# Performance work log

Measured on AMD Instinct MI355X. Metric: run time of the kernel, lower is better.

## Reference

```python
import jax, jax.numpy as jnp
import numpy as np

B, N, D, P, H, DH = 1, 1536, 512, 64, 16, 64
INNER = H * DH  # 1024

def _ln(x, g, b, eps=1e-5):
    m = jnp.mean(x, axis=-1, keepdims=True)
    v = jnp.var(x, axis=-1, keepdims=True)
    return (x - m) / jnp.sqrt(v + eps) * g + b

def setup_inputs() -> dict:
    key = jax.random.key(0)
    ks = jax.random.split(key, 10)
    s = 0.02
    return {
        "node_feats": jax.random.normal(ks[0], (B, N, D), jnp.float32),
        "pair_feats": jax.random.normal(ks[1], (B, N, N, P), jnp.float32),
        "mask": jnp.ones((B, N, N), dtype=bool),
        "ln_node_g": jnp.ones((D,), jnp.float32), "ln_node_b": jnp.zeros((D,), jnp.float32),
        "ln_pair_g": jnp.ones((P,), jnp.float32), "ln_pair_b": jnp.zeros((P,), jnp.float32),
        "Wq": s * jax.random.normal(ks[2], (D, INNER), jnp.float32),
        "bq": jnp.zeros((INNER,), jnp.float32),
        "Wkv": s * jax.random.normal(ks[3], (D, 2 * INNER), jnp.float32),
        "bkv": jnp.zeros((2 * INNER,), jnp.float32),
        "qln_g": jnp.ones((INNER,), jnp.float32), "qln_b": jnp.zeros((INNER,), jnp.float32),
        "kln_g": jnp.ones((INNER,), jnp.float32), "kln_b": jnp.zeros((INNER,), jnp.float32),
        "Wg": s * jax.random.normal(ks[4], (D, INNER), jnp.float32),
        "bg": jnp.zeros((INNER,), jnp.float32),
        "Wbias": s * jax.random.normal(ks[5], (P, H), jnp.float32),
        "Wout": s * jax.random.normal(ks[6], (INNER, D), jnp.float32),
        "bout": jnp.zeros((D,), jnp.float32),
        "n_queries": 0,
        "n_keys": 0,
    }

def reference(node_feats, pair_feats, mask, ln_node_g, ln_node_b, ln_pair_g, ln_pair_b,
              Wq, bq, Wkv, bkv, qln_g, qln_b, kln_g, kln_b, Wg, bg, Wbias, Wout, bout,
              n_queries, n_keys):
    b, n, _ = node_feats.shape
    x = _ln(node_feats, ln_node_g, ln_node_b)          # [b,n,D]
    p = _ln(pair_feats, ln_pair_g, ln_pair_b)          # [b,n,n,P]
    q = _ln(x @ Wq + bq, qln_g, qln_b)                 # [b,n,I]
    kv = x @ Wkv + bkv
    k, v = jnp.split(kv, 2, axis=-1)
    k = _ln(k, kln_g, kln_b)
    g = x @ Wg + bg                                    # gating, [b,n,I]
    bias = jnp.einsum('bijp,ph->bhij', p, Wbias)       # pair bias, [b,h,n,n]
    # split heads -> [b,h,n,dh]
    split = lambda t: t.reshape(b, n, H, DH).transpose(0, 2, 1, 3)
    qh, kh, vh, gh = split(q), split(k), split(v), split(g)
    scale = DH ** -0.5
    sim = jnp.einsum('bhid,bhjd->bhij', qh, kh) * scale
    sim = jnp.where(mask[:, None, :, :], sim, jnp.finfo(sim.dtype).min)
    attn = jax.nn.softmax(sim + bias, axis=-1)
    o = jnp.einsum('bhij,bhjd->bhid', attn, vh)        # [b,h,n,dh]
    o = jax.nn.sigmoid(gh) * o
    o = o.transpose(0, 2, 1, 3).reshape(b, n, INNER)
    return o @ Wout + bout
```

## Files before the change

kernel.cpp:

```cpp
#include <hip/hip_runtime.h>

#define NN 1536
#define DD 512
#define PP 64
#define HH 16
#define DHD 64
#define INNER 1024
#define NCHUNK 4
#define JT_PER 6

typedef __attribute__((ext_vector_type(4))) float f32x4;
typedef __attribute__((ext_vector_type(8))) _Float16 f16x8;
typedef __attribute__((ext_vector_type(4))) _Float16 f16x4;

__device__ inline float wave_sum(float v) {
#pragma unroll
  for (int m = 1; m <= 32; m <<= 1) v += __shfl_xor(v, m);
  return v;
}

__global__ __launch_bounds__(256) void prep_kernel(const float* __restrict__ Wq,
    const float* __restrict__ Wkv, const float* __restrict__ Wg,
    const float* __restrict__ Wout, const float* __restrict__ nf,
    const float* __restrict__ lng, const float* __restrict__ lnb,
    _Float16* __restrict__ BTall, _Float16* __restrict__ WoutT,
    _Float16* __restrict__ x16) {
  int bid = blockIdx.x;
  int tid = threadIdx.x;
  if (bid >= 640) {
    int i = bid - 640;
    int c = tid * 2;
    float2 v = *(const float2*)&nf[(size_t)i * DD + c];
    float s = v.x + v.y, ss = v.x * v.x + v.y * v.y;
    s = wave_sum(s); ss = wave_sum(ss);
    __shared__ float red[2][4];
    int w = tid >> 6;
    if ((tid & 63) == 0) { red[0][w] = s; red[1][w] = ss; }
    __syncthreads();
    s = red[0][0] + red[0][1] + red[0][2] + red[0][3];
    ss = red[1][0] + red[1][1] + red[1][2] + red[1][3];
    float mean = s * (1.f / DD);
    float var = ss * (1.f / DD) - mean * mean;
    float rstd = rsqrtf(var + 1e-5f);
    x16[(size_t)i * DD + c + 0] = (_Float16)((v.x - mean) * rstd * lng[c + 0] + lnb[c + 0]);
    x16[(size_t)i * DD + c + 1] = (_Float16)((v.y - mean) * rstd * lng[c + 1] + lnb[c + 1]);
    return;
  }
  const float* src; int Cs, c0, r0, outStride, outCol; _Float16* dst;
  if (bid < 512) {
    int x = bid & 63, y = bid >> 6;
    int cg0 = x * 64; r0 = y * 64;
    if (cg0 < 1024)      { src = Wq;  Cs = 1024; c0 = cg0; }
    else if (cg0 < 3072) { src = Wkv; Cs = 2048; c0 = cg0 - 1024; }
    else                 { src = Wg;  Cs = 1024; c0 = cg0 - 3072; }
    dst = BTall; outStride = DD; outCol = cg0;
  } else {
    int b = bid - 512;
    int x = b & 7, y = b >> 3;
    c0 = x * 64; r0 = y * 64;
    src = Wout; Cs = DD; dst = WoutT; outStride = INNER; outCol = c0;
  }
  __shared__ float tile[64][65];
  int ri = tid >> 4, ci = (tid & 15) * 4;
#pragma unroll
  for (int p = 0; p < 4; ++p) {
    float4 v = *(const float4*)&src[(size_t)(r0 + ri + p * 16) * Cs + c0 + ci];
    tile[ri + p * 16][ci + 0] = v.x;
    tile[ri + p * 16][ci + 1] = v.y;
    tile[ri + p * 16][ci + 2] = v.z;
    tile[ri + p * 16][ci + 3] = v.w;
  }
  __syncthreads();
  int wr = tid >> 3, wc = (tid & 7) * 8;
#pragma unroll
  for (int p = 0; p < 2; ++p) {
    f16x8 o;
#pragma unroll
    for (int jj = 0; jj < 8; ++jj) o[jj] = (_Float16)tile[wc + jj][wr + p * 32];
    *(f16x8*)&dst[(size_t)(outCol + wr + p * 32) * outStride + r0 + wc] = o;
  }
}

__device__ __forceinline__ void pb_body(int i, int q, int tid,
    const float* __restrict__ pair, const float* __restrict__ pg,
    const float* __restrict__ pb, const float* __restrict__ Wbias,
    _Float16* __restrict__ bias16) {
  int lane = tid & 63, w = tid >> 6;
  int lj = lane & 15, pbase = (lane >> 4) * 8;
  const int off0 = 0, off1 = 4, off2 = 32, off3 = 36;
  f16x8 wb0, wb1;
#pragma unroll
  for (int jj = 0; jj < 8; ++jj) {
    wb0[jj] = (_Float16)Wbias[(pbase + jj) * HH + lj];
    wb1[jj] = (_Float16)Wbias[(pbase + 32 + jj) * HH + lj];
  }
  f32x4 gv0 = *(const f32x4*)&pg[pbase + off0], gv1 = *(const f32x4*)&pg[pbase + off1];
  f32x4 gv2 = *(const f32x4*)&pg[pbase + off2], gv3 = *(const f32x4*)&pg[pbase + off3];
  f32x4 bb0 = *(const f32x4*)&pb[pbase + off0], bb1 = *(const f32x4*)&pb[pbase + off1];
  f32x4 bb2 = *(const f32x4*)&pb[pbase + off2], bb3 = *(const f32x4*)&pb[pbase + off3];
  __shared__ _Float16 trans[2][16][72];
  int jbase = q * 384 + w * 16 + lj;
  const float* srcp = &pair[((size_t)i * NN + jbase) * PP];
  f32x4 v0 = *(const f32x4*)&srcp[pbase + off0];
  f32x4 v1 = *(const f32x4*)&srcp[pbase + off1];
  f32x4 v2 = *(const f32x4*)&srcp[pbase + off2];
  f32x4 v3 = *(const f32x4*)&srcp[pbase + off3];
  for (int t = 0; t < 6; ++t) {
    int jt0 = q * 384 + t * 64;
    f32x4 n0, n1, n2, n3;
    if (t < 5) {
      const float* ns = &pair[((size_t)i * NN + jbase + (t + 1) * 64) * PP];
      n0 = *(const f32x4*)&ns[pbase + off0];
      n1 = *(const f32x4*)&ns[pbase + off1];
      n2 = *(const f32x4*)&ns[pbase + off2];
      n3 = *(const f32x4*)&ns[pbase + off3];
    }
    float s = 0.f, ss = 0.f;
#pragma unroll
    for (int e = 0; e < 4; ++e) {
      s += v0[e] + v1[e] + v2[e] + v3[e];
      ss += v0[e] * v0[e] + v1[e] * v1[e] + v2[e] * v2[e] + v3[e] * v3[e];
    }
    s += __shfl_xor(s, 16); s += __shfl_xor(s, 32);
    ss += __shfl_xor(ss, 16); ss += __shfl_xor(ss, 32);
    float mean = s * (1.f / PP);
    float var = ss * (1.f / PP) - mean * mean;
    float rstd = rsqrtf(var + 1e-5f);
    f16x8 a0, a1;
#pragma unroll
    for (int e = 0; e < 4; ++e) {
      a0[e]     = (_Float16)((v0[e] - mean) * rstd * gv0[e] + bb0[e]);
      a0[4 + e] = (_Float16)((v1[e] - mean) * rstd * gv1[e] + bb1[e]);
      a1[e]     = (_Float16)((v2[e] - mean) * rstd * gv2[e] + bb2[e]);
      a1[4 + e] = (_Float16)((v3[e] - mean) * rstd * gv3[e] + bb3[e]);
    }
    f32x4 cacc = {};
    cacc = __builtin_amdgcn_mfma_f32_16x16x32_f16(a0, wb0, cacc, 0, 0, 0);
    cacc = __builtin_amdgcn_mfma_f32_16x16x32_f16(a1, wb1, cacc, 0, 0, 0);
#pragma unroll
    for (int rg = 0; rg < 4; ++rg)
      trans[t & 1][lj][w * 16 + (lane >> 4) * 4 + rg] = (_Float16)cacc[rg];
    __syncthreads();
    int hh = tid >> 4, jc = (tid & 15) * 4;
    f16x4 ov = *(const f16x4*)&trans[t & 1][hh][jc];
    *(f16x4*)&bias16[((size_t)hh * NN + i) * NN + jt0 + jc] = ov;
    v0 = n0; v1 = n1; v2 = n2; v3 = n3;
  }
}

__device__ __forceinline__ void gemm_proj_body(int m0, int n0, int tid,
    const _Float16* __restrict__ A, const _Float16* __restrict__ BT,
    const float* __restrict__ bq, const float* __restrict__ bkv,
    const float* __restrict__ bg, _Float16* __restrict__ C) {
  __shared__ _Float16 As[64][72];
  __shared__ _Float16 Bs[64][72];
  int lane = tid & 63, w = tid >> 6;
  int wm = (w & 1) * 32, wn = (w >> 1) * 32;
  f32x4 acc[2][2] = {};
  int r = tid >> 3, c8 = (tid & 7) * 8;
  int lr = lane & 15, lg = lane >> 4;
  for (int k0 = 0; k0 < DD; k0 += 64) {
    *(f16x8*)&As[r][c8]      = *(const f16x8*)&A[(size_t)(m0 + r) * DD + k0 + c8];
    *(f16x8*)&As[r + 32][c8] = *(const f16x8*)&A[(size_t)(m0 + r + 32) * DD + k0 + c8];
    *(f16x8*)&Bs[r][c8]      = *(const f16x8*)&BT[(size_t)(n0 + r) * DD + k0 + c8];
    *(f16x8*)&Bs[r + 32][c8] = *(const f16x8*)&BT[(size_t)(n0 + r + 32) * DD + k0 + c8];
    __syncthreads();
#pragma unroll
    for (int kf = 0; kf < 2; ++kf) {
      f16x8 a0 = *(const f16x8*)&As[wm + lr][kf * 32 + lg * 8];
      f16x8 a1 = *(const f16x8*)&As[wm + 16 + lr][kf * 32 + lg * 8];
      f16x8 b0 = *(const f16x8*)&Bs[wn + lr][kf * 32 + lg * 8];
      f16x8 b1 = *(const f16x8*)&Bs[wn + 16 + lr][kf * 32 + lg * 8];
      acc[0][0] = __builtin_amdgcn_mfma_f32_16x16x32_f16(a0, b0, acc[0][0], 0, 0, 0);
      acc[0][1] = __builtin_amdgcn_mfma_f32_16x16x32_f16(a0, b1, acc[0][1], 0, 0, 0);
      acc[1][0] = __builtin_amdgcn_mfma_f32_16x16x32_f16(a1, b0, acc[1][0], 0, 0, 0);
      acc[1][1] = __builtin_amdgcn_mfma_f32_16x16x32_f16(a1, b1, acc[1][1], 0, 0, 0);
    }
    __syncthreads();
  }
#pragma unroll
  for (int mi = 0; mi < 2; ++mi)
#pragma unroll
    for (int ni = 0; ni < 2; ++ni)
#pragma unroll
      for (int rg = 0; rg < 4; ++rg) {
        int row = m0 + wm + mi * 16 + lg * 4 + rg;
        int col = n0 + wn + ni * 16 + lr;
        float bv = (col < 1024) ? bq[col] : (col < 3072) ? bkv[col - 1024] : bg[col - 3072];
        C[(size_t)row * 4096 + col] = (_Float16)(acc[mi][ni][rg] + bv);
      }
}

__device__ __forceinline__ void qkv_body(int i, int tid,
    const _Float16* __restrict__ prebuf,
    const float* __restrict__ qg, const float* __restrict__ qb,
    const float* __restrict__ kg, const float* __restrict__ kb,
    _Float16* __restrict__ q16, _Float16* __restrict__ k16) {
  int c = tid * 4;
  const _Float16* rowp = &prebuf[(size_t)i * 4096];
  f16x4 qh = *(const f16x4*)&rowp[c];
  f16x4 kh = *(const f16x4*)&rowp[1024 + c];
  float qv[4], kv[4];
#pragma unroll
  for (int e = 0; e < 4; ++e) { qv[e] = (float)qh[e]; kv[e] = (float)kh[e]; }
  float qs = qv[0] + qv[1] + qv[2] + qv[3];
  float qss = qv[0] * qv[0] + qv[1] * qv[1] + qv[2] * qv[2] + qv[3] * qv[3];
  float ks = kv[0] + kv[1] + kv[2] + kv[3];
  float kss = kv[0] * kv[0] + kv[1] * kv[1] + kv[2] * kv[2] + kv[3] * kv[3];
  qs = wave_sum(qs); qss = wave_sum(qss); ks = wave_sum(ks); kss = wave_sum(kss);
  __shared__ float red[4][4];
  int w = tid >> 6;
  if ((tid & 63) == 0) { red[0][w] = qs; red[1][w] = qss; red[2][w] = ks; red[3][w] = kss; }
  __syncthreads();
  qs = red[0][0] + red[0][1] + red[0][2] + red[0][3];
  qss = red[1][0] + red[1][1] + red[1][2] + red[1][3];
  ks = red[2][0] + red[2][1] + red[2][2] + red[2][3];
  kss = red[3][0] + red[3][1] + red[3][2] + red[3][3];
  float qm = qs * (1.f / INNER), qvr = qss * (1.f / INNER) - qm * qm, qr = rsqrtf(qvr + 1e-5f);
  float km = ks * (1.f / INNER), kvr = kss * (1.f / INNER) - km * km, kr = rsqrtf(kvr + 1e-5f);
  int hh = c >> 6, d = c & 63;
  size_t offo = ((size_t)hh * NN + i) * DHD + d;
  f16x4 qo, ko;
#pragma unroll
  for (int e = 0; e < 4; ++e) {
    qo[e] = (_Float16)((qv[e] - qm) * qr * qg[c + e] + qb[c + e]);
    ko[e] = (_Float16)((kv[e] - km) * kr * kg[c + e] + kb[c + e]);
  }
  *(f16x4*)&q16[offo] = qo;
  *(f16x4*)&k16[offo] = ko;
}

__device__ __forceinline__ void vt_body(int t, int tid,
    const _Float16* __restrict__ prebuf, _Float16* __restrict__ vT16) {
  int z = t / 24, y = t - z * 24;
  __shared__ _Float16 tile[64][72];
  int r0 = y * 64;
  int ri = tid >> 3, ci = (tid & 7) * 8;
#pragma unroll
  for (int p = 0; p < 2; ++p)
    *(f16x8*)&tile[ri + p * 32][ci] =
        *(const f16x8*)&prebuf[(size_t)(r0 + ri + p * 32) * 4096 + 2048 + z * 64 + ci];
  __syncthreads();
#pragma unroll
  for (int p = 0; p < 2; ++p) {
    f16x8 o;
#pragma unroll
    for (int jj = 0; jj < 8; ++jj) o[jj] = tile[ci + jj][ri + p * 32];
    *(f16x8*)&vT16[((size_t)z * DHD + ri + p * 32) * NN + r0 + ci] = o;
  }
}

__device__ __forceinline__ void attn_core(int it, int h, int ck, int tid,
    const _Float16* __restrict__ q16, const _Float16* __restrict__ k16,
    const _Float16* __restrict__ vT16, const _Float16* __restrict__ bias16,
    f32x4 oacc[4], float& mOut, float& lOut) {
  int lane = tid & 63, w = tid >> 6;
  int lr = lane & 15, lg = lane >> 4;
  __shared__ _Float16 Kt[64][72];
  __shared__ _Float16 Vt[64][72];
  int ib0 = it * 64;
  int ib = ib0 + w * 16;
  f16x8 qb0 = *(const f16x8*)&q16[((size_t)h * NN + ib + lr) * DHD + lg * 8];
  f16x8 qb1 = *(const f16x8*)&q16[((size_t)h * NN + ib + lr) * DHD + 32 + lg * 8];
  float m = -INFINITY, lsum = 0.f;
  int sr = tid >> 3, sc = (tid & 7) * 8;
  int jt0g = ck * JT_PER;
  const _Float16* brow = &bias16[((size_t)h * NN + ib + lr) * NN];
  f16x8 kA, kB, vA, vB;
  {
    int j0 = jt0g * 64;
    kA = *(const f16x8*)&k16[((size_t)h * NN + j0 + sr) * DHD + sc];
    kB = *(const f16x8*)&k16[((size_t)h * NN + j0 + sr + 32) * DHD + sc];
    vA = *(const f16x8*)&vT16[((size_t)h * DHD + sr) * NN + j0 + sc];
    vB = *(const f16x8*)&vT16[((size_t)h * DHD + sr + 32) * NN + j0 + sc];
  }
  for (int jj = 0; jj < JT_PER; ++jj) {
    int j0 = (jt0g + jj) * 64;
    *(f16x8*)&Kt[sr][sc] = kA;
    *(f16x8*)&Kt[sr + 32][sc] = kB;
    *(f16x8*)&Vt[sr][sc] = vA;
    *(f16x8*)&Vt[sr + 32][sc] = vB;
    f16x4 bl[4];
#pragma unroll
    for (int jq = 0; jq < 4; ++jq)
      bl[jq] = *(const f16x4*)&brow[j0 + jq * 16 + lg * 4];
    __syncthreads();
    if (jj + 1 < JT_PER) {
      int j1 = j0 + 64;
      kA = *(const f16x8*)&k16[((size_t)h * NN + j1 + sr) * DHD + sc];
      kB = *(const f16x8*)&k16[((size_t)h * NN + j1 + sr + 32) * DHD + sc];
      vA = *(const f16x8*)&vT16[((size_t)h * DHD + sr) * NN + j1 + sc];
      vB = *(const f16x8*)&vT16[((size_t)h * DHD + sr + 32) * NN + j1 + sc];
    }
    float s[4][4];
#pragma unroll
    for (int jq = 0; jq < 4; ++jq) {
      f16x8 ka0 = *(const f16x8*)&Kt[jq * 16 + lr][lg * 8];
      f16x8 ka1 = *(const f16x8*)&Kt[jq * 16 + lr][32 + lg * 8];
      f32x4 c = {};
      c = __builtin_amdgcn_mfma_f32_16x16x32_f16(ka0, qb0, c, 0, 0, 0);
      c = __builtin_amdgcn_mfma_f32_16x16x32_f16(ka1, qb1, c, 0, 0, 0);
#pragma unroll
      for (int r = 0; r < 4; ++r)
        s[jq][r] = c[r] * 0.125f + (float)bl[jq][r];
    }
    float tmax = s[0][0];
#pragma unroll
    for (int jq = 0; jq < 4; ++jq)
#pragma unroll
      for (int r = 0; r < 4; ++r) tmax = fmaxf(tmax, s[jq][r]);
    tmax = fmaxf(tmax, __shfl_xor(tmax, 16));
    tmax = fmaxf(tmax, __shfl_xor(tmax, 32));
    float mn = fmaxf(m, tmax);
    float alpha = __expf(m - mn);
    float ps = 0.f;
    f16x4 pf[4];
#pragma unroll
    for (int jq = 0; jq < 4; ++jq)
#pragma unroll
      for (int r = 0; r < 4; ++r) {
        float p = __expf(s[jq][r] - mn);
        ps += p;
        pf[jq][r] = (_Float16)p;
      }
    ps += __shfl_xor(ps, 16);
    ps += __shfl_xor(ps, 32);
    lsum = lsum * alpha + ps;
    m = mn;
    float ar[4];
#pragma unroll
    for (int r = 0; r < 4; ++r) ar[r] = __shfl(alpha, lg * 4 + r);
#pragma unroll
    for (int dt = 0; dt < 4; ++dt)
#pragma unroll
      for (int r = 0; r < 4; ++r) oacc[dt][r] *= ar[r];
#pragma unroll
    for (int dt = 0; dt < 4; ++dt)
#pragma unroll
      for (int jq = 0; jq < 4; ++jq) {
        f16x4 vb = *(const f16x4*)&Vt[dt * 16 + lr][jq * 16 + lg * 4];
        oacc[dt] = __builtin_amdgcn_mfma_f32_16x16x16f16(pf[jq], vb, oacc[dt], 0, 0, 0);
      }
    __syncthreads();
  }
  mOut = m;
  lOut = lsum;
}

__device__ __forceinline__ void attn_body(int it, int h, int ck, int tid,
    const _Float16* __restrict__ q16, const _Float16* __restrict__ k16,
    const _Float16* __restrict__ vT16, const _Float16* __restrict__ bias16,
    _Float16* __restrict__ opart, float* __restrict__ mlbuf) {
  int lane = tid & 63, w = tid >> 6;
  int lr = lane & 15, lg = lane >> 4;
  f32x4 oacc[4] = {};
  float m, lsum;
  attn_core(it, h, ck, tid, q16, k16, vT16, bias16, oacc, m, lsum);
  size_t pbase = (((size_t)it * HH + h) * NCHUNK + ck) * 4096 + (size_t)w * 1024;
#pragma unroll
  for (int dt = 0; dt < 4; ++dt) {
    f16x4 ov;
#pragma unroll
    for (int r = 0; r < 4; ++r) ov[r] = (_Float16)oacc[dt][r];
    *(f16x4*)&opart[pbase + dt * 256 + lane * 4] = ov;
  }
  if (lg == 0) {
    size_t mb = (((size_t)it * HH + h) * NCHUNK + ck) * 128;
    mlbuf[mb + w * 16 + lr] = m;
    mlbuf[mb + 64 + w * 16 + lr] = lsum;
  }
}

__global__ __launch_bounds__(256) void fat2(const float* __restrict__ pair,
    const float* __restrict__ pg, const float* __restrict__ pb,
    const float* __restrict__ Wbias, _Float16* __restrict__ bias16,
    const _Float16* __restrict__ x16, const _Float16* __restrict__ BTall,
    const float* __restrict__ bq, const float* __restrict__ bkv,
    const float* __restrict__ bg, _Float16* __restrict__ prebuf16) {
  int bid = blockIdx.x;
  int g = bid / 3, r = bid - g * 3;
  int tid = threadIdx.x;
  if (r == 2) {
    gemm_proj_body((g >> 6) * 64, (g & 63) * 64, tid, x16, BTall, bq, bkv, bg, prebuf16);
  } else {
    int p = g * 2 + r;
    pb_body(p % NN, p / NN, tid, pair, pg, pb, Wbias, bias16);
  }
}

__global__ __launch_bounds__(256) void fat3(const float* __restrict__ pair,
    const float* __restrict__ pg, const float* __restrict__ pb,
    const float* __restrict__ Wbias, _Float16* __restrict__ bias16,
    const _Float16* __restrict__ prebuf16,
    const float* __restrict__ qg, const float* __restrict__ qb,
    const float* __restrict__ kg, const float* __restrict__ kb,
    _Float16* __restrict__ q16, _Float16* __restrict__ k16,
    _Float16* __restrict__ vT16) {
  int bid = blockIdx.x;
  int g = bid / 9, r = bid - g * 9;
  int tid = threadIdx.x;
  if (r < 4) {
    pb_body(g * 4 + r, 2, tid, pair, pg, pb, Wbias, bias16);
  } else if (r < 8) {
    qkv_body(g * 4 + (r - 4), tid, prebuf16, qg, qb, kg, kb, q16, k16);
  } else {
    vt_body(g, tid, prebuf16, vT16);
  }
}

__global__ __launch_bounds__(256) void fat4(const float* __restrict__ pair,
    const float* __restrict__ pg, const float* __restrict__ pb,
    const float* __restrict__ Wbias, _Float16* __restrict__ bias16,
    const _Float16* __restrict__ q16, const _Float16* __restrict__ k16,
    const _Float16* __restrict__ vT16, _Float16* __restrict__ opart,
    float* __restrict__ mlbuf) {
  int bid = blockIdx.x;
  int g = bid / 7, r = bid - g * 7;
  int tid = threadIdx.x;
  if (r < 4) {
    pb_body(g * 4 + r, 3, tid, pair, pg, pb, Wbias, bias16);
  } else {
    int a = g * 3 + (r - 4);
    int ck = a % 3, h = (a / 3) % 16, it = a / 48;
    attn_body(it, h, ck, tid, q16, k16, vT16, bias16, opart, mlbuf);
  }
}

__global__ __launch_bounds__(256) void attn_final(const _Float16* __restrict__ q16,
    const _Float16* __restrict__ k16, const _Float16* __restrict__ vT16,
    const _Float16* __restrict__ bias16, const _Float16* __restrict__ opart,
    const float* __restrict__ mlbuf, const _Float16* __restrict__ prebuf,
    _Float16* __restrict__ o16) {
  int it = blockIdx.x, h = blockIdx.y;
  int tid = threadIdx.x, lane = tid & 63, w = tid >> 6;
  int lr = lane & 15, lg = lane >> 4;
  f32x4 oacc[4] = {};
  float m3, l3;
  attn_core(it, h, 3, tid, q16, k16, vT16, bias16, oacc, m3, l3);
  float mc[NCHUNK], lc[NCHUNK];
#pragma unroll
  for (int c = 0; c < 3; ++c) {
    size_t mb = (((size_t)it * HH + h) * NCHUNK + c) * 128;
    mc[c] = mlbuf[mb + w * 16 + lr];
    lc[c] = mlbuf[mb + 64 + w * 16 + lr];
  }
  mc[3] = m3; lc[3] = l3;
  float mg = fmaxf(fmaxf(mc[0], mc[1]), fmaxf(mc[2], mc[3]));
  float wcc[NCHUNK], lt = 0.f;
#pragma unroll
  for (int c = 0; c < NCHUNK; ++c) {
    wcc[c] = __expf(mc[c] - mg);
    lt += wcc[c] * lc[c];
  }
  float wq[NCHUNK][4], ltq[4];
#pragma unroll
  for (int r = 0; r < 4; ++r) {
    ltq[r] = __shfl(lt, lg * 4 + r);
#pragma unroll
    for (int c = 0; c < NCHUNK; ++c) wq[c][r] = __shfl(wcc[c], lg * 4 + r);
  }
#pragma unroll
  for (int dt = 0; dt < 4; ++dt) {
    float o[4];
#pragma unroll
    for (int r = 0; r < 4; ++r) o[r] = wq[3][r] * oacc[dt][r];
#pragma unroll
    for (int c = 0; c < 3; ++c) {
      size_t base = (((size_t)it * HH + h) * NCHUNK + c) * 4096 + (size_t)w * 1024;
      f16x4 v = *(const f16x4*)&opart[base + dt * 256 + lane * 4];
#pragma unroll
      for (int r = 0; r < 4; ++r) o[r] += wq[c][r] * (float)v[r];
    }
    int d = dt * 16 + lr;
#pragma unroll
    for (int r = 0; r < 4; ++r) {
      int i = it * 64 + w * 16 + lg * 4 + r;
      float gt = (float)prebuf[(size_t)i * 4096 + 3072 + h * DHD + d];
      float val = o[r] / ltq[r] * (1.f / (1.f + __expf(-gt)));
      o16[(size_t)i * INNER + h * DHD + d] = (_Float16)val;
    }
  }
}

__global__ __launch_bounds__(256) void gemm_f16(const _Float16* __restrict__ A,
    const _Float16* __restrict__ BT, const float* __restrict__ bias,
    float* __restrict__ C, int M, int N, int K) {
  __shared__ _Float16 As[64][72];
  __shared__ _Float16 Bs[64][72];
  int tid = threadIdx.x, lane = tid & 63, w = tid >> 6;
  int m0 = blockIdx.y * 64, n0 = blockIdx.x * 64;
  int wm = (w & 1) * 32, wn = (w >> 1) * 32;
  f32x4 acc[2][2] = {};
  int r = tid >> 3, c8 = (tid & 7) * 8;
  int lr = lane & 15, lg = lane >> 4;
  for (int k0 = 0; k0 < K; k0 += 64) {
    *(f16x8*)&As[r][c8]      = *(const f16x8*)&A[(size_t)(m0 + r) * K + k0 + c8];
    *(f16x8*)&As[r + 32][c8] = *(const f16x8*)&A[(size_t)(m0 + r + 32) * K + k0 + c8];
    *(f16x8*)&Bs[r][c8]      = *(const f16x8*)&BT[(size_t)(n0 + r) * K + k0 + c8];
    *(f16x8*)&Bs[r + 32][c8] = *(const f16x8*)&BT[(size_t)(n0 + r + 32) * K + k0 + c8];
    __syncthreads();
#pragma unroll
    for (int kf = 0; kf < 2; ++kf) {
      f16x8 a0 = *(const f16x8*)&As[wm + lr][kf * 32 + lg * 8];
      f16x8 a1 = *(const f16x8*)&As[wm + 16 + lr][kf * 32 + lg * 8];
      f16x8 b0 = *(const f16x8*)&Bs[wn + lr][kf * 32 + lg * 8];
      f16x8 b1 = *(const f16x8*)&Bs[wn + 16 + lr][kf * 32 + lg * 8];
      acc[0][0] = __builtin_amdgcn_mfma_f32_16x16x32_f16(a0, b0, acc[0][0], 0, 0, 0);
      acc[0][1] = __builtin_amdgcn_mfma_f32_16x16x32_f16(a0, b1, acc[0][1], 0, 0, 0);
      acc[1][0] = __builtin_amdgcn_mfma_f32_16x16x32_f16(a1, b0, acc[1][0], 0, 0, 0);
      acc[1][1] = __builtin_amdgcn_mfma_f32_16x16x32_f16(a1, b1, acc[1][1], 0, 0, 0);
    }
    __syncthreads();
  }
#pragma unroll
  for (int mi = 0; mi < 2; ++mi)
#pragma unroll
    for (int ni = 0; ni < 2; ++ni)
#pragma unroll
      for (int rg = 0; rg < 4; ++rg) {
        int row = m0 + wm + mi * 16 + lg * 4 + rg;
        int col = n0 + wn + ni * 16 + lr;
        C[(size_t)row * N + col] = acc[mi][ni][rg] + bias[col];
      }
}

extern "C" void kernel_launch(void* const* d_in, const int* in_sizes, int n_in,
                              void* d_out, int out_size, void* d_ws, size_t ws_size,
                              hipStream_t stream) {
  const float* node  = (const float*)d_in[0];
  const float* pair  = (const float*)d_in[1];
  const float* ln_ng = (const float*)d_in[3];
  const float* ln_nb = (const float*)d_in[4];
  const float* ln_pg = (const float*)d_in[5];
  const float* ln_pb = (const float*)d_in[6];
  const float* Wq    = (const float*)d_in[7];
  const float* bq    = (const float*)d_in[8];
  const float* Wkv   = (const float*)d_in[9];
  const float* bkv   = (const float*)d_in[10];
  const float* qlg   = (const float*)d_in[11];
  const float* qlb   = (const float*)d_in[12];
  const float* klg   = (const float*)d_in[13];
  const float* klb   = (const float*)d_in[14];
  const float* Wg    = (const float*)d_in[15];
  const float* bg    = (const float*)d_in[16];
  const float* Wbias = (const float*)d_in[17];
  const float* Wout  = (const float*)d_in[18];
  const float* bout  = (const float*)d_in[19];
  float* out = (float*)d_out;

  char* ws = (char*)d_ws;
  const size_t MB = 1u << 20;
  _Float16* BTall    = (_Float16*)(ws + 0 * MB);
  _Float16* WoutT    = (_Float16*)(ws + 4 * MB);
  _Float16* x16      = (_Float16*)(ws + 5 * MB);
  _Float16* prebuf16 = (_Float16*)(ws + 8 * MB);
  _Float16* q16      = (_Float16*)(ws + 20 * MB);
  _Float16* k16      = (_Float16*)(ws + 23 * MB);
  _Float16* vT16     = (_Float16*)(ws + 29 * MB);
  _Float16* o16      = (_Float16*)(ws + 32 * MB);
  _Float16* bias16   = (_Float16*)(ws + 36 * MB);
  _Float16* opart    = (_Float16*)(ws + 112 * MB);
  float*    mlbuf    = (float*)(ws + 126 * MB);

  prep_kernel<<<640 + NN, 256, 0, stream>>>(Wq, Wkv, Wg, Wout, node, ln_ng, ln_nb,
                                            BTall, WoutT, x16);
  fat2<<<4608, 256, 0, stream>>>(pair, ln_pg, ln_pb, Wbias, bias16,
                                 x16, BTall, bq, bkv, bg, prebuf16);
  fat3<<<3456, 256, 0, stream>>>(pair, ln_pg, ln_pb, Wbias, bias16,
                                 prebuf16, qlg, qlb, klg, klb, q16, k16, vT16);
  fat4<<<2688, 256, 0, stream>>>(pair, ln_pg, ln_pb, Wbias, bias16,
                                 q16, k16, vT16, opart, mlbuf);
  attn_final<<<dim3(NN / 64, HH), 256, 0, stream>>>(q16, k16, vT16, bias16,
                                                    opart, mlbuf, prebuf16, o16);
  gemm_f16<<<dim3(DD / 64, NN / 64), 256, 0, stream>>>(o16, WoutT, bout, out, NN, DD, INNER);
}
```

Before: 242.0 us.

## Overlap pair-bias chunk with prep stage by fusing into new fat1 kernel

Turns the weight-transpose and node-layernorm prep kernel into a device function and interleaves it with pair-bias blocks in a new fat1 launch. Pair-bias chunk 0 now runs alongside prep instead of inside fat2, and fat2 shrinks to pair-bias chunk 1 plus the projection GEMM. The aim is to spread the memory-bound pair-feature streaming over more stages so it overlaps the short prep work. This rebalances the work across the pipeline. Correctness depends on the 128*29 block grid covering all 2176 prep blocks and 1536 bias rows exactly.

```diff
diff --git a/kernel.cpp b/kernel.cpp
--- a/kernel.cpp
+++ b/kernel.cpp
@@ -19,16 +19,14 @@
   return v;
 }
 
-__global__ __launch_bounds__(256) void prep_kernel(const float* __restrict__ Wq,
-    const float* __restrict__ Wkv, const float* __restrict__ Wg,
-    const float* __restrict__ Wout, const float* __restrict__ nf,
-    const float* __restrict__ lng, const float* __restrict__ lnb,
-    _Float16* __restrict__ BTall, _Float16* __restrict__ WoutT,
-    _Float16* __restrict__ x16) {
-  int bid = blockIdx.x;
-  int tid = threadIdx.x;
-  if (bid >= 640) {
-    int i = bid - 640;
+__device__ __forceinline__ void prep_body(int pid, int tid,
+    const float* __restrict__ Wq, const float* __restrict__ Wkv,
+    const float* __restrict__ Wg, const float* __restrict__ Wout,
+    const float* __restrict__ nf, const float* __restrict__ lng,
+    const float* __restrict__ lnb, _Float16* __restrict__ BTall,
+    _Float16* __restrict__ WoutT, _Float16* __restrict__ x16) {
+  if (pid >= 640) {
+    int i = pid - 640;
     int c = tid * 2;
     float2 v = *(const float2*)&nf[(size_t)i * DD + c];
     float s = v.x + v.y, ss = v.x * v.x + v.y * v.y;
@@ -47,15 +45,15 @@
     return;
   }
   const float* src; int Cs, c0, r0, outStride, outCol; _Float16* dst;
-  if (bid < 512) {
-    int x = bid & 63, y = bid >> 6;
+  if (pid < 512) {
+    int x = pid & 63, y = pid >> 6;
     int cg0 = x * 64; r0 = y * 64;
     if (cg0 < 1024)      { src = Wq;  Cs = 1024; c0 = cg0; }
     else if (cg0 < 3072) { src = Wkv; Cs = 2048; c0 = cg0 - 1024; }
     else                 { src = Wg;  Cs = 1024; c0 = cg0 - 3072; }
     dst = BTall; outStride = DD; outCol = cg0;
   } else {
-    int b = bid - 512;
+    int b = pid - 512;
     int x = b & 7, y = b >> 3;
     c0 = x * 64; r0 = y * 64;
     src = Wout; Cs = DD; dst = WoutT; outStride = INNER; outCol = c0;
@@ -371,6 +369,25 @@
   }
 }
 
+__global__ __launch_bounds__(256) void fat1(const float* __restrict__ Wq,
+    const float* __restrict__ Wkv, const float* __restrict__ Wg,
+    const float* __restrict__ Wout, const float* __restrict__ nf,
+    const float* __restrict__ lng, const float* __restrict__ lnb,
+    _Float16* __restrict__ BTall, _Float16* __restrict__ WoutT,
+    _Float16* __restrict__ x16,
+    const float* __restrict__ pair, const float* __restrict__ pg,
+    const float* __restrict__ pb, const float* __restrict__ Wbias,
+    _Float16* __restrict__ bias16) {
+  int bid = blockIdx.x;
+  int g = bid / 29, r = bid - g * 29;
+  int tid = threadIdx.x;
+  if (r < 17) {
+    prep_body(g * 17 + r, tid, Wq, Wkv, Wg, Wout, nf, lng, lnb, BTall, WoutT, x16);
+  } else {
+    pb_body(g * 12 + (r - 17), 0, tid, pair, pg, pb, Wbias, bias16);
+  }
+}
+
 __global__ __launch_bounds__(256) void fat2(const float* __restrict__ pair,
     const float* __restrict__ pg, const float* __restrict__ pb,
     const float* __restrict__ Wbias, _Float16* __restrict__ bias16,
@@ -378,13 +395,12 @@
     const float* __restrict__ bq, const float* __restrict__ bkv,
     const float* __restrict__ bg, _Float16* __restrict__ prebuf16) {
   int bid = blockIdx.x;
-  int g = bid / 3, r = bid - g * 3;
+  int g = bid >> 1, r = bid & 1;
   int tid = threadIdx.x;
-  if (r == 2) {
+  if (r == 1) {
     gemm_proj_body((g >> 6) * 64, (g & 63) * 64, tid, x16, BTall, bq, bkv, bg, prebuf16);
   } else {
-    int p = g * 2 + r;
-    pb_body(p % NN, p / NN, tid, pair, pg, pb, Wbias, bias16);
+    pb_body(g, 1, tid, pair, pg, pb, Wbias, bias16);
   }
 }
 
@@ -562,9 +578,10 @@
   _Float16* opart    = (_Float16*)(ws + 112 * MB);
   float*    mlbuf    = (float*)(ws + 126 * MB);
 
-  prep_kernel<<<640 + NN, 256, 0, stream>>>(Wq, Wkv, Wg, Wout, node, ln_ng, ln_nb,
-                                            BTall, WoutT, x16);
-  fat2<<<4608, 256, 0, stream>>>(pair, ln_pg, ln_pb, Wbias, bias16,
+  fat1<<<3712, 256, 0, stream>>>(Wq, Wkv, Wg, Wout, node, ln_ng, ln_nb,
+                                 BTall, WoutT, x16,
+                                 pair, ln_pg, ln_pb, Wbias, bias16);
+  fat2<<<3072, 256, 0, stream>>>(pair, ln_pg, ln_pb, Wbias, bias16,
                                  x16, BTall, bq, bkv, bg, prebuf16);
   fat3<<<3456, 256, 0, stream>>>(pair, ln_pg, ln_pb, Wbias, bias16,
                                  prebuf16, qlg, qlb, klg, klb, q16, k16, vT16);
```

Result: slower. 249.8 us (+3.2%).
